# Kernel tuning notes

Measured on AMD Instinct MI355X. Metric: run time of the kernel, lower is better.

The kernel has to match this reference:

```python
import jax, jax.numpy as jnp
import numpy as np

EPS = 1e-6
K_MEM, C_MEM = 512, 2048
SEQ, BATCH = 256, 16
NUM_LAYERS, NUM_HEADS, HEAD_DIM = 12, 12, 64
KV_DIM = NUM_LAYERS * NUM_HEADS * HEAD_DIM * 2  # 18432
NOISE_STD = 0.01
PINV_STEPS = 3
BEN_COHEN_INIT = -5.0


def approx_pinv(A, steps=PINV_STEPS):
    # Ben-Cohen iterative pseudoinverse. A: (B, M, N) -> (B, N, M)
    alpha = jnp.minimum(jnp.exp(jnp.float32(BEN_COHEN_INIT)), jnp.float32(5e-4))  # clamp(max=5e-4)
    P = alpha * jnp.swapaxes(A, -2, -1)
    for _ in range(steps):
        P = 2.0 * P - (P @ A) @ P  # matches bmm(bmm(P, A), P)
    return P


def setup_inputs() -> dict:
    key = jax.random.key(0)
    ks = jax.random.split(key, 6)
    lim = np.sqrt(6.0 / (C_MEM + KV_DIM))  # xavier_uniform
    return {
        "z_sequence": jax.random.normal(ks[0], (SEQ, BATCH, C_MEM), jnp.float32),
        "z_query": jax.random.normal(ks[1], (BATCH, C_MEM), jnp.float32),
        "noise": jax.random.normal(ks[2], (SEQ, BATCH, C_MEM), jnp.float32),
        "memory_mean": jax.random.normal(ks[3], (K_MEM, C_MEM), jnp.float32) * 0.02,
        "memory_logvar": jnp.zeros((K_MEM,), jnp.float32),
        "w_logvar": jnp.zeros((1,), jnp.float32),
        "W_M_weight": jax.random.uniform(ks[4], (KV_DIM, C_MEM), jnp.float32, -lim, lim),
    }


def reference(z_sequence, z_query, noise, memory_mean, memory_logvar, w_logvar, W_M_weight):
    B = z_query.shape[0]
    # ---- write ----
    prior_var = jnp.exp(memory_logvar) + EPS                     # (K,)
    prior_mean_b = jnp.broadcast_to(memory_mean, (B, K_MEM, C_MEM))
    z_noise = z_sequence + noise * NOISE_STD                     # (S, B, C)
    z_t = jnp.swapaxes(z_noise, 0, 1)                            # (B, S, C)
    M_pinv = approx_pinv(prior_mean_b)                           # (B, C, K)
    w = z_t @ M_pinv                                             # (B, S, K)
    w_pinv = approx_pinv(w)                                      # (B, K, S)
    new_memory_mean = w_pinv @ z_t                               # (B, K, C)
    # KL divergence (post_var == prior_var here)
    t1 = C_MEM * jnp.sum(prior_var / prior_var)
    t2 = jnp.sum((new_memory_mean - prior_mean_b) ** 2 / prior_var[None, :, None], axis=(-2, -1))
    t3 = -jnp.float32(C_MEM * K_MEM)
    t4 = C_MEM * jnp.sum(jnp.log(prior_var) - jnp.log(prior_var))
    dkl_M = jnp.mean(t1 + t2 + t3 + t4)
    # ---- read (deterministic addressing) ----
    M_pinv2 = approx_pinv(new_memory_mean)                       # (B, C, K)
    w_mean = jnp.einsum('bc,bck->bk', z_query, M_pinv2)          # (B, K)
    z_retrieved = jnp.einsum('bk,bkc->bc', w_mean, new_memory_mean)  # (B, C)
    Z_r_kv = z_retrieved @ W_M_weight.T                          # (B, kv_dim)
    wl = jnp.broadcast_to(w_logvar, w_mean.shape)
    dkl_w = 0.5 * jnp.sum(jnp.exp(wl) + w_mean ** 2 - 1.0 - wl)
    return z_retrieved, Z_r_kv, dkl_M, dkl_w
```

## Files before the change

### kernel.cpp

```cpp
#include <hip/hip_runtime.h>

#define ALPHA 5.0e-4f

typedef short s16x8 __attribute__((ext_vector_type(8)));
typedef unsigned short u16x8 __attribute__((ext_vector_type(8)));
typedef unsigned short u16x4 __attribute__((ext_vector_type(4)));
typedef float f32x4 __attribute__((ext_vector_type(4)));

__device__ __forceinline__ unsigned short f2bf(float f) {
    unsigned int u = __builtin_bit_cast(unsigned int, f);
    u += 0x7fffu + ((u >> 16) & 1u);
    return (unsigned short)(u >> 16);
}
__device__ __forceinline__ float bf2f(unsigned short h) {
    return __builtin_bit_cast(float, (unsigned int)h << 16);
}
__device__ __forceinline__ f32x4 mfma16(s16x8 a, s16x8 b, f32x4 c) {
    return __builtin_amdgcn_mfma_f32_16x16x32_bf16(a, b, c, 0, 0, 0);
}

__device__ __forceinline__ void prefetch_chunk(const float* __restrict__ WM,
                                               int chunk, int tid)
{
    const float4* wp = (const float4*)WM + (long long)chunk * 12288;
    float4 s = {0.f, 0.f, 0.f, 0.f};
#pragma unroll 8
    for (int i = 0; i < 48; ++i) {
        const float4 v = wp[tid + i * 256];
        s.x += v.x; s.y += v.y; s.z += v.z; s.w += v.w;
    }
    asm volatile("" :: "v"(s.x), "v"(s.y), "v"(s.z), "v"(s.w));
}

template<int ROWS>
__device__ __forceinline__ void stage_kcontig(const float* __restrict__ src, int ld,
                                              unsigned short* __restrict__ lds, int tid)
{
#pragma unroll
    for (int it = 0; it < ROWS * 8 / 256; ++it) {
        const int g = tid + it * 256;
        const int row = g >> 3, s = g & 7;
        const float* p = src + (long long)row * ld + s * 8;
        const float4 x0 = *(const float4*)p;
        const float4 x1 = *(const float4*)(p + 4);
        u16x8 h;
        h[0] = f2bf(x0.x); h[1] = f2bf(x0.y); h[2] = f2bf(x0.z); h[3] = f2bf(x0.w);
        h[4] = f2bf(x1.x); h[5] = f2bf(x1.y); h[6] = f2bf(x1.z); h[7] = f2bf(x1.w);
        *(u16x8*)(lds + row * 64 + ((s ^ (row & 7)) << 3)) = h;
    }
}

template<int ROWS>
__device__ __forceinline__ void stage_kstrided(const float* __restrict__ src, int ld,
                                               unsigned short* __restrict__ lds, int tid)
{
    constexpr int KPT = ROWS * 64 / 256;
    const int m = tid % ROWS, kb = (tid / ROWS) * KPT;
#pragma unroll
    for (int j8 = 0; j8 < KPT / 8; ++j8) {
        u16x8 h;
#pragma unroll
        for (int j = 0; j < 8; ++j)
            h[j] = f2bf(src[(long long)(kb + j8 * 8 + j) * ld + m]);
        const int s = (kb >> 3) + j8;
        *(u16x8*)(lds + m * 64 + ((s ^ (m & 7)) << 3)) = h;
    }
}

template<int ROWS>
__device__ __forceinline__ void stage_kcontig_b(const unsigned short* __restrict__ src, int ld,
                                                unsigned short* __restrict__ lds, int tid)
{
#pragma unroll
    for (int it = 0; it < ROWS * 8 / 256; ++it) {
        const int g = tid + it * 256;
        const int row = g >> 3, s = g & 7;
        const u16x8 h = *(const u16x8*)(src + (long long)row * ld + s * 8);
        *(u16x8*)(lds + row * 64 + ((s ^ (row & 7)) << 3)) = h;
    }
}

template<int ROWS>
__device__ __forceinline__ void stage_kstrided_b(const unsigned short* __restrict__ src, int ld,
                                                 unsigned short* __restrict__ lds, int tid)
{
    constexpr int KPT = ROWS * 64 / 256;
    const int m = tid % ROWS, kb = (tid / ROWS) * KPT;
#pragma unroll
    for (int j8 = 0; j8 < KPT / 8; ++j8) {
        u16x8 h;
#pragma unroll
        for (int j = 0; j < 8; ++j)
            h[j] = src[(long long)(kb + j8 * 8 + j) * ld + m];
        const int s = (kb >> 3) + j8;
        *(u16x8*)(lds + m * 64 + ((s ^ (m & 7)) << 3)) = h;
    }
}

template<int BM, int BN, bool TA, bool TB>
__device__ __forceinline__
void gemm_dev_f32(int bx, int by,
                  const float* __restrict__ A, int lda,
                  const float* __restrict__ B, int ldb,
                  float* __restrict__ D, int ldd, int Kd)
{
    constexpr int TWM = BM / 2, TWN = BN / 2;
    constexpr int FM = TWM / 16, FN = TWN / 16;
    __shared__ unsigned short As[BM * 64];
    __shared__ unsigned short Bs[BN * 64];

    const int tid = threadIdx.x;
    const int lane = tid & 63, w = tid >> 6;
    const int wm = w >> 1, wn = w & 1;
    const int lrow = lane & 15, lk = lane >> 4;
    const int m0 = by * BM, n0 = bx * BN;

    f32x4 acc[FM][FN];
#pragma unroll
    for (int i = 0; i < FM; ++i)
#pragma unroll
        for (int j = 0; j < FN; ++j) acc[i][j] = (f32x4){0.f, 0.f, 0.f, 0.f};

    for (int k0 = 0; k0 < Kd; k0 += 64) {
        if (!TA) stage_kcontig<BM>(A + (long long)m0 * lda + k0, lda, As, tid);
        else     stage_kstrided<BM>(A + (long long)k0 * lda + m0, lda, As, tid);
        if (TB)  stage_kcontig<BN>(B + (long long)n0 * ldb + k0, ldb, Bs, tid);
        else     stage_kstrided<BN>(B + (long long)k0 * ldb + n0, ldb, Bs, tid);
        __syncthreads();
#pragma unroll
        for (int kk = 0; kk < 2; ++kk) {
            s16x8 ah[FM], bh[FN];
#pragma unroll
            for (int i = 0; i < FM; ++i) {
                const int row = wm * TWM + i * 16 + lrow;
                const int s = kk * 4 + lk;
                ah[i] = *(const s16x8*)(As + row * 64 + ((s ^ (row & 7)) << 3));
            }
#pragma unroll
            for (int j = 0; j < FN; ++j) {
                const int col = wn * TWN + j * 16 + lrow;
                const int s = kk * 4 + lk;
                bh[j] = *(const s16x8*)(Bs + col * 64 + ((s ^ (col & 7)) << 3));
            }
#pragma unroll
            for (int i = 0; i < FM; ++i)
#pragma unroll
                for (int j = 0; j < FN; ++j)
                    acc[i][j] = mfma16(ah[i], bh[j], acc[i][j]);
        }
        __syncthreads();
    }

#pragma unroll
    for (int i = 0; i < FM; ++i)
#pragma unroll
        for (int j = 0; j < FN; ++j) {
            const int col = n0 + wn * TWN + j * 16 + lrow;
#pragma unroll
            for (int r = 0; r < 4; ++r) {
                const int row = m0 + wm * TWM + i * 16 + lk * 4 + r;
                D[(long long)row * ldd + col] = acc[i][j][r];
            }
        }
}

__global__ __launch_bounds__(256)
void fused_prep_kernel(const float* __restrict__ zs, const float* __restrict__ no,
                       const float* __restrict__ zq, const float* __restrict__ mm,
                       unsigned short* __restrict__ ztb, float* __restrict__ q,
                       float* __restrict__ Gp)
{
    const int blk = blockIdx.x, t = threadIdx.x;
    if (blk % 9 == 8) {
        const int g = blk / 9;
        const int ky = g & 7;
        const int tile = g >> 3;
        gemm_dev_f32<64, 64, false, true>(
            tile & 7, tile >> 3,
            mm + ky * 256, 2048, mm + ky * 256, 2048,
            Gp + (long long)ky * 262144, 512, 256);
    } else {
        const int bs = blk - blk / 9;
        const int b = bs >> 8, sI = bs & 255;
        const long long in = ((long long)sI * 16 + b) * 2048 + t * 8;
        const f32x4 z0 = __builtin_nontemporal_load((const f32x4*)(zs + in));
        const f32x4 z1 = __builtin_nontemporal_load((const f32x4*)(zs + in + 4));
        const f32x4 n0 = __builtin_nontemporal_load((const f32x4*)(no + in));
        const f32x4 n1 = __builtin_nontemporal_load((const f32x4*)(no + in + 4));
        float zf[8];
#pragma unroll
        for (int j = 0; j < 4; ++j) {
            zf[j]     = fmaf(0.01f, n0[j], z0[j]);
            zf[j + 4] = fmaf(0.01f, n1[j], z1[j]);
        }
        u16x8 o;
#pragma unroll
        for (int j = 0; j < 8; ++j) o[j] = f2bf(zf[j]);
        *(u16x8*)(ztb + ((long long)bs * 2048 + t * 8)) = o;
        const float4 q0 = *(const float4*)(zq + b * 2048 + t * 8);
        const float4 q1 = *(const float4*)(zq + b * 2048 + t * 8 + 4);
        float qa = zf[0] * q0.x + zf[1] * q0.y + zf[2] * q0.z + zf[3] * q0.w
                 + zf[4] * q1.x + zf[5] * q1.y + zf[6] * q1.z + zf[7] * q1.w;
        __shared__ float red[256];
        red[t] = qa; __syncthreads();
        for (int st = 128; st > 0; st >>= 1) { if (t < st) red[t] += red[t + st]; __syncthreads(); }
        if (t == 0) q[bs] = red[0];
    }
}

__global__ __launch_bounds__(256)
void vg_kernel(const unsigned short* __restrict__ ztb, const float* __restrict__ mm,
               const float* __restrict__ Gp, const float* __restrict__ WM,
               unsigned short* __restrict__ Vb, unsigned short* __restrict__ G1b,
               float* __restrict__ wmean, float* __restrict__ out)
{
    const int blk = blockIdx.x, tid = threadIdx.x;
    if (blk < 512) {
        constexpr int BM = 64, BN = 64, TWM = 32, TWN = 32, FM = 2, FN = 2;
        __shared__ unsigned short As[BM * 64];
        __shared__ unsigned short Bs[BN * 64];
        const int r = blk & 7, t = blk >> 3;
        const int by = r + 8 * (t & 7), bx = t >> 3;
        const int lane = tid & 63, w = tid >> 6;
        const int wm = w >> 1, wn = w & 1;
        const int lrow = lane & 15, lk = lane >> 4;
        const int m0 = by * BM, n0 = bx * BN;

        f32x4 acc[FM][FN];
#pragma unroll
        for (int i = 0; i < FM; ++i)
#pragma unroll
            for (int j = 0; j < FN; ++j) acc[i][j] = (f32x4){0.f, 0.f, 0.f, 0.f};

        for (int k0 = 0; k0 < 2048; k0 += 64) {
            stage_kcontig_b<BM>(ztb + (long long)m0 * 2048 + k0, 2048, As, tid);
            stage_kcontig<BN>(mm + (long long)n0 * 2048 + k0, 2048, Bs, tid);
            __syncthreads();
#pragma unroll
            for (int kk = 0; kk < 2; ++kk) {
                s16x8 ah[FM], bh[FN];
#pragma unroll
                for (int i = 0; i < FM; ++i) {
                    const int row = wm * TWM + i * 16 + lrow;
                    const int s = kk * 4 + lk;
                    ah[i] = *(const s16x8*)(As + row * 64 + ((s ^ (row & 7)) << 3));
                }
#pragma unroll
                for (int j = 0; j < FN; ++j) {
                    const int col = wn * TWN + j * 16 + lrow;
                    const int s = kk * 4 + lk;
                    bh[j] = *(const s16x8*)(Bs + col * 64 + ((s ^ (col & 7)) << 3));
                }
#pragma unroll
                for (int i = 0; i < FM; ++i)
#pragma unroll
                    for (int j = 0; j < FN; ++j)
                        acc[i][j] = mfma16(ah[i], bh[j], acc[i][j]);
            }
            __syncthreads();
        }

#pragma unroll
        for (int i = 0; i < FM; ++i)
#pragma unroll
            for (int j = 0; j < FN; ++j) {
                const int col = n0 + wn * TWN + j * 16 + lrow;
#pragma unroll
                for (int rr = 0; rr < 4; ++rr) {
                    const int row = m0 + wm * TWM + i * 16 + lk * 4 + rr;
                    Vb[(long long)row * 512 + col] = f2bf(acc[i][j][rr]);
                }
            }
    } else if (blk < 768) {
        const int idx = (blk - 512) * 256 + tid;
        f32x4 s = {0.f, 0.f, 0.f, 0.f};
#pragma unroll
        for (int p = 0; p < 8; ++p) {
            const f32x4 v = *(const f32x4*)(Gp + (long long)p * 262144 + idx * 4);
            s[0] += v[0]; s[1] += v[1]; s[2] += v[2]; s[3] += v[3];
        }
        u16x4 h;
#pragma unroll
        for (int j = 0; j < 4; ++j) h[j] = f2bf(s[j]);
        *(u16x4*)(G1b + idx * 4) = h;
    } else if (blk < 777) {
        const int zb = blk - 768;
        float4* oz = (float4*)(out + 32768);
        const int base = (zb * 256 + tid) * 32;
#pragma unroll
        for (int i = 0; i < 32; ++i) oz[base + i] = (float4){0.f, 0.f, 0.f, 0.f};
        if (zb == 0) {
            float4* wm4 = (float4*)wmean;
            for (int i = tid; i < 2048; i += 256) wm4[i] = (float4){0.f, 0.f, 0.f, 0.f};
            if (tid == 0) out[327680] = 0.f;
        }
    } else {
        prefetch_chunk(WM, blk - 777, tid);
    }
}

__global__ __launch_bounds__(256)
void wT2_kernel(const unsigned short* __restrict__ Vb,
                const unsigned short* __restrict__ G1b,
                unsigned short* __restrict__ wTb,
                const float* __restrict__ q, float* __restrict__ wmean)
{
    constexpr int BM = 64, BN = 64, TWM = 32, TWN = 32, FM = 2, FN = 2;
    __shared__ unsigned short As[BM * 64];
    __shared__ unsigned short Bs[BN * 64];
    const int lin = blockIdx.x;
    const int r = lin & 7, t = lin >> 3;
    const int by = r + 8 * (t & 7), bx = t >> 3;
    const int tid = threadIdx.x;
    const int lane = tid & 63, w = tid >> 6;
    const int wm = w >> 1, wn = w & 1;
    const int lrow = lane & 15, lk = lane >> 4;
    const int m0 = by * BM, n0 = bx * BN;

    f32x4 acc[FM][FN];
#pragma unroll
    for (int i = 0; i < FM; ++i)
#pragma unroll
        for (int j = 0; j < FN; ++j) acc[i][j] = (f32x4){0.f, 0.f, 0.f, 0.f};

    for (int k0 = 0; k0 < 512; k0 += 64) {
        stage_kcontig_b<BM>(Vb + (long long)m0 * 512 + k0, 512, As, tid);
        stage_kcontig_b<BN>(G1b + (long long)n0 * 512 + k0, 512, Bs, tid);
        __syncthreads();
#pragma unroll
        for (int kk = 0; kk < 2; ++kk) {
            s16x8 ah[FM], bh[FN];
#pragma unroll
            for (int i = 0; i < FM; ++i) {
                const int row = wm * TWM + i * 16 + lrow;
                const int s = kk * 4 + lk;
                ah[i] = *(const s16x8*)(As + row * 64 + ((s ^ (row & 7)) << 3));
            }
#pragma unroll
            for (int j = 0; j < FN; ++j) {
                const int col = wn * TWN + j * 16 + lrow;
                const int s = kk * 4 + lk;
                bh[j] = *(const s16x8*)(Bs + col * 64 + ((s ^ (col & 7)) << 3));
            }
#pragma unroll
            for (int i = 0; i < FM; ++i)
#pragma unroll
                for (int j = 0; j < FN; ++j)
                    acc[i][j] = mfma16(ah[i], bh[j], acc[i][j]);
        }
        __syncthreads();
    }

    const float a8 = 8.0f * ALPHA, a28 = -28.0f * ALPHA * ALPHA;
    float up[FN] = {0.f, 0.f};
#pragma unroll
    for (int i = 0; i < FM; ++i)
#pragma unroll
        for (int rr = 0; rr < 4; ++rr) {
            const int row = m0 + wm * TWM + i * 16 + lk * 4 + rr;
            const float qv = q[row];
#pragma unroll
            for (int j = 0; j < FN; ++j) {
                const int col = n0 + wn * TWN + j * 16 + lrow;
                const float v = fmaf(a8, bf2f(Vb[(long long)row * 512 + col]),
                                     a28 * acc[i][j][rr]);
                wTb[(long long)(row >> 8) * 131072 + (long long)col * 256 + (row & 255)] = f2bf(v);
                up[j] = fmaf(v, qv, up[j]);
            }
        }
    const int b = m0 >> 8;
#pragma unroll
    for (int j = 0; j < FN; ++j) {
        float v = up[j];
        v += __shfl_xor(v, 16);
        v += __shfl_xor(v, 32);
        if (lk == 0) {
            const int col = n0 + wn * TWN + j * 16 + lrow;
            atomicAdd(&wmean[b * 512 + col], (64.0f * ALPHA * ALPHA) * v);
        }
    }
}

__global__ __launch_bounds__(256)
void tail1_kernel(const unsigned short* __restrict__ wTb,
                  const unsigned short* __restrict__ ztb,
                  const float* __restrict__ wmean, const float* __restrict__ wlv,
                  const float* __restrict__ WM, float* __restrict__ out)
{
    __shared__ __align__(16) float smemf[1024];
    const int blk = blockIdx.x, tid = threadIdx.x;
    if (blk < 256) {
        float* wms = smemf;
        float* ys  = smemf + 512;
        float* red2 = smemf + 768;
        const int r8 = blk & 7, t8 = blk >> 3;
        const int b = r8 + 8 * (t8 & 1), ct = t8 >> 1;
        wms[tid] = wmean[b * 512 + tid];
        wms[tid + 256] = wmean[b * 512 + 256 + tid];
        __syncthreads();
        {
            const unsigned short* wp = wTb + (long long)b * 131072 + tid;
            float yv = 0.f;
#pragma unroll 8
            for (int k = 0; k < 512; ++k)
                yv = fmaf(wms[k], bf2f(wp[(long long)k * 256]), yv);
            ys[tid] = yv;
        }
        __syncthreads();
        const int c = ct * 128 + (tid & 127), sh = tid >> 7;
        const unsigned short* zp = ztb + (long long)b * 524288 + c;
        float acc2 = 0.f;
        const int sbase = sh * 128;
#pragma unroll 8
        for (int s = 0; s < 128; ++s)
            acc2 = fmaf(ys[sbase + s], bf2f(zp[(long long)(sbase + s) * 2048]), acc2);
        red2[tid] = acc2; __syncthreads();
        if (sh == 0)
            out[(long long)b * 2048 + c] = (8.0f * ALPHA) * (red2[tid] + red2[tid + 128]);
    } else if (blk == 256) {
        float* red = smemf;
        float s = 0.f;
        for (int i = tid; i < 16 * 512; i += 256) { const float v = wmean[i]; s += v * v; }
        red[tid] = s; __syncthreads();
        for (int st = 128; st > 0; st >>= 1) { if (tid < st) red[tid] += red[tid + st]; __syncthreads(); }
        if (tid == 0) {
            const float l = wlv[0];
            out[327681] = 0.5f * (red[0] + 8192.0f * (expf(l) - 1.0f - l));
        }
    } else {
        prefetch_chunk(WM, 512 + (blk - 257), tid);
    }
}

__global__ __launch_bounds__(256)
void tail2_kernel(const unsigned short* __restrict__ wTb,
                  const unsigned short* __restrict__ ztb,
                  const float* __restrict__ mm, const float* __restrict__ mlv,
                  const float* __restrict__ WM, float* __restrict__ out)
{
    __shared__ __align__(16) unsigned char smem[34304];
    const int g = blockIdx.x, tid = threadIdx.x;
    const int grp = g / 26, p = g % 26;
    if (p < 8) {
        constexpr int BM = 128, BN = 128, TWM = 64, TWN = 64, FM = 4, FN = 4;
        unsigned short* As = (unsigned short*)smem;
        unsigned short* Bs = As + BM * 64;
        float* ivars = (float*)(smem + 32768);
        float* red = (float*)(smem + 33280);
        const int bz = ((2 * grp + p) & 7) + 8 * (grp & 1);
        const int rest = grp >> 1;
        const int by = rest & 3, bx = rest >> 2;
        const int lane = tid & 63, w = tid >> 6;
        const int wm = w >> 1, wn = w & 1;
        const int lrow = lane & 15, lk = lane >> 4;
        const int m0 = by * BM, n0 = bx * BN;

        if (tid < 128) ivars[tid] = 1.0f / (expf(mlv[m0 + tid]) + 1e-6f);

        f32x4 acc[FM][FN];
#pragma unroll
        for (int i = 0; i < FM; ++i)
#pragma unroll
            for (int j = 0; j < FN; ++j) acc[i][j] = (f32x4){0.f, 0.f, 0.f, 0.f};

        for (int k0 = 0; k0 < 256; k0 += 64) {
            stage_kcontig_b<BM>(wTb + (long long)bz * 131072 + (long long)m0 * 256 + k0, 256, As, tid);
            stage_kstrided_b<BN>(ztb + (long long)bz * 524288 + (long long)k0 * 2048 + n0, 2048, Bs, tid);
            __syncthreads();
#pragma unroll
            for (int kk = 0; kk < 2; ++kk) {
                s16x8 ah[FM], bh[FN];
#pragma unroll
                for (int i = 0; i < FM; ++i) {
                    const int row = wm * TWM + i * 16 + lrow;
                    const int s = kk * 4 + lk;
                    ah[i] = *(const s16x8*)(As + row * 64 + ((s ^ (row & 7)) << 3));
                }
#pragma unroll
                for (int j = 0; j < FN; ++j) {
                    const int col = wn * TWN + j * 16 + lrow;
                    const int s = kk * 4 + lk;
                    bh[j] = *(const s16x8*)(Bs + col * 64 + ((s ^ (col & 7)) << 3));
                }
#pragma unroll
                for (int i = 0; i < FM; ++i)
#pragma unroll
                    for (int j = 0; j < FN; ++j)
                        acc[i][j] = mfma16(ah[i], bh[j], acc[i][j]);
            }
            __syncthreads();
        }

        const float A8 = 8.0f * ALPHA;
        float da = 0.f;
#pragma unroll
        for (int i = 0; i < FM; ++i)
#pragma unroll
            for (int j = 0; j < FN; ++j) {
                const int cl = wn * TWN + j * 16 + lrow;
#pragma unroll
                for (int rr = 0; rr < 4; ++rr) {
                    const int rl = wm * TWM + i * 16 + lk * 4 + rr;
                    const float v = A8 * acc[i][j][rr];
                    const float d = v - mm[(long long)(m0 + rl) * 2048 + (n0 + cl)];
                    da = fmaf(d * d, ivars[rl], da);
                }
            }
        red[tid] = da; __syncthreads();
        for (int st = 128; st > 0; st >>= 1) { if (tid < st) red[tid] += red[tid + st]; __syncthreads(); }
        if (tid == 0) atomicAdd(&out[327680], red[0] * (1.0f / 16.0f));
    } else {
        const int z = grp * 18 + (p - 8);
        const int bx = z % 288, ky = z / 288;
        const int lane = tid & 63, w = tid >> 6;
        const int d0 = bx * 64 + w * 16;
        const int kc0 = ky * 256;
        const int rr = lane & 15, kq = lane >> 4;
        const float* zr = out;
        s16x8 areg[8];
        const float* zb = zr + rr * 2048 + kc0 + kq * 8;
#pragma unroll
        for (int s = 0; s < 8; ++s) {
            const f32x4 a0 = *(const f32x4*)(zb + s * 32);
            const f32x4 a1 = *(const f32x4*)(zb + s * 32 + 4);
            u16x8 h;
#pragma unroll
            for (int j = 0; j < 4; ++j) { h[j] = f2bf(a0[j]); h[j + 4] = f2bf(a1[j]); }
            areg[s] = __builtin_bit_cast(s16x8, h);
        }
        f32x4 acc = {0.f, 0.f, 0.f, 0.f};
        const float* wb = WM + (long long)(d0 + rr) * 2048 + kc0 + kq * 8;
#pragma unroll
        for (int s = 0; s < 8; ++s) {
            const f32x4 b0 = *(const f32x4*)(wb + s * 32);
            const f32x4 b1 = *(const f32x4*)(wb + s * 32 + 4);
            u16x8 h;
#pragma unroll
            for (int j = 0; j < 4; ++j) { h[j] = f2bf(b0[j]); h[j + 4] = f2bf(b1[j]); }
            acc = mfma16(areg[s], __builtin_bit_cast(s16x8, h), acc);
        }
        float* oz = out + 32768;
#pragma unroll
        for (int r = 0; r < 4; ++r)
            atomicAdd(&oz[(long long)(kq * 4 + r) * 18432 + d0 + rr], acc[r]);
    }
}

extern "C" void kernel_launch(void* const* d_in, const int* in_sizes, int n_in,
                              void* d_out, int out_size, void* d_ws, size_t ws_size,
                              hipStream_t stream)
{
    (void)in_sizes; (void)n_in; (void)out_size; (void)ws_size;
    const float* z_seq   = (const float*)d_in[0];
    const float* z_query = (const float*)d_in[1];
    const float* noise   = (const float*)d_in[2];
    const float* mm      = (const float*)d_in[3];
    const float* mlv     = (const float*)d_in[4];
    const float* wlv     = (const float*)d_in[5];
    const float* WM      = (const float*)d_in[6];
    float* out = (float*)d_out;

    char* wsb = (char*)d_ws;
    unsigned short* ztb  = (unsigned short*)(wsb);
    unsigned short* wTb  = (unsigned short*)(wsb + (16LL << 20));
    float*          Gp   = (float*)(wsb + (24LL << 20));
    unsigned short* G1b  = (unsigned short*)(wsb + (32LL << 20));
    unsigned short* Vb   = (unsigned short*)(wsb + (33LL << 20));
    float*          qvec = (float*)(wsb + (38LL << 20));
    float*          wmean = (float*)(wsb + (39LL << 20));

    fused_prep_kernel<<<4608, 256, 0, stream>>>(z_seq, noise, z_query, mm,
                                                ztb, qvec, Gp);
    vg_kernel<<<1289, 256, 0, stream>>>(ztb, mm, Gp, WM, Vb, G1b, wmean, out);
    wT2_kernel<<<512, 256, 0, stream>>>(Vb, G1b, wTb, qvec, wmean);
    tail1_kernel<<<513, 256, 0, stream>>>(wTb, ztb, wmean, wlv, WM, out);
    tail2_kernel<<<3328, 256, 0, stream>>>(wTb, ztb, mm, mlv, WM, out);
}
```

Measured before the change: 160.0 us.

## Compute w_mean algebraically from V and G1 to fuse wT GEMM with retrieval

Instead of waiting for the full wT matrix before computing w_mean, w_mean is derived from the product u=V^T q, which vg_kernel now accumulates with atomics. A small mid_kernel then applies G1 to get w_mean, the KL term, and a vector h. This lets the wT GEMM and the first retrieval projection (now V·h, computed from V directly) run concurrently in one launch, taking the wT→tail1 dependency off the critical path. In exchange it adds a small, poorly parallel 16-block kernel and changes floating-point summation order.

```diff
diff --git a/kernel.cpp b/kernel.cpp
--- a/kernel.cpp
+++ b/kernel.cpp
@@ -168,9 +168,14 @@
 void fused_prep_kernel(const float* __restrict__ zs, const float* __restrict__ no,
                        const float* __restrict__ zq, const float* __restrict__ mm,
                        unsigned short* __restrict__ ztb, float* __restrict__ q,
-                       float* __restrict__ Gp)
+                       float* __restrict__ Gp, float* __restrict__ uVb)
 {
     const int blk = blockIdx.x, t = threadIdx.x;
+    if (blk == 4608) {
+        float4* u4 = (float4*)uVb;
+        for (int i = t; i < 2048; i += 256) u4[i] = (float4){0.f, 0.f, 0.f, 0.f};
+        return;
+    }
     if (blk % 9 == 8) {
         const int g = blk / 9;
         const int ky = g & 7;
@@ -211,8 +216,9 @@
 __global__ __launch_bounds__(256)
 void vg_kernel(const unsigned short* __restrict__ ztb, const float* __restrict__ mm,
                const float* __restrict__ Gp, const float* __restrict__ WM,
+               const float* __restrict__ q,
                unsigned short* __restrict__ Vb, unsigned short* __restrict__ G1b,
-               float* __restrict__ wmean, float* __restrict__ out)
+               float* __restrict__ uVb, float* __restrict__ out)
 {
     const int blk = blockIdx.x, tid = threadIdx.x;
     if (blk < 512) {
@@ -260,17 +266,32 @@
             __syncthreads();
         }
 
+        float up[FN] = {0.f, 0.f};
 #pragma unroll
         for (int i = 0; i < FM; ++i)
 #pragma unroll
-            for (int j = 0; j < FN; ++j) {
+            for (int rr = 0; rr < 4; ++rr) {
+                const int row = m0 + wm * TWM + i * 16 + lk * 4 + rr;
+                const float qv = q[row];
+#pragma unroll
+                for (int j = 0; j < FN; ++j) {
+                    const int col = n0 + wn * TWN + j * 16 + lrow;
+                    const float v = acc[i][j][rr];
+                    Vb[(long long)row * 512 + col] = f2bf(v);
+                    up[j] = fmaf(v, qv, up[j]);
+                }
+            }
+        const int b = m0 >> 8;
+#pragma unroll
+        for (int j = 0; j < FN; ++j) {
+            float v = up[j];
+            v += __shfl_xor(v, 16);
+            v += __shfl_xor(v, 32);
+            if (lk == 0) {
                 const int col = n0 + wn * TWN + j * 16 + lrow;
-#pragma unroll
-                for (int rr = 0; rr < 4; ++rr) {
-                    const int row = m0 + wm * TWM + i * 16 + lk * 4 + rr;
-                    Vb[(long long)row * 512 + col] = f2bf(acc[i][j][rr]);
-                }
-            }
+                atomicAdd(&uVb[b * 512 + col], v);
+            }
+        }
     } else if (blk < 768) {
         const int idx = (blk - 512) * 256 + tid;
         f32x4 s = {0.f, 0.f, 0.f, 0.f};
@@ -289,122 +310,152 @@
         const int base = (zb * 256 + tid) * 32;
 #pragma unroll
         for (int i = 0; i < 32; ++i) oz[base + i] = (float4){0.f, 0.f, 0.f, 0.f};
-        if (zb == 0) {
-            float4* wm4 = (float4*)wmean;
-            for (int i = tid; i < 2048; i += 256) wm4[i] = (float4){0.f, 0.f, 0.f, 0.f};
-            if (tid == 0) out[327680] = 0.f;
-        }
+        if (zb == 0 && tid == 0) { out[327680] = 0.f; out[327681] = 0.f; }
     } else {
         prefetch_chunk(WM, blk - 777, tid);
     }
 }
 
+__global__ __launch_bounds__(512)
+void mid_kernel(const unsigned short* __restrict__ G1b, const float* __restrict__ uVb,
+                const float* __restrict__ wlv, float* __restrict__ hbuf,
+                float* __restrict__ out)
+{
+    __shared__ float uVs[512], wms[512], red[512];
+    const int b = blockIdx.x, k = threadIdx.x;
+    uVs[k] = uVb[b * 512 + k];
+    __syncthreads();
+    const unsigned short* grow = G1b + (long long)k * 512;
+    float g1 = 0.f;
+#pragma unroll 4
+    for (int j = 0; j < 512; j += 8) {
+        const u16x8 gv = *(const u16x8*)(grow + j);
+#pragma unroll
+        for (int jj = 0; jj < 8; ++jj) g1 = fmaf(bf2f(gv[jj]), uVs[j + jj], g1);
+    }
+    const float a8 = 8.0f * ALPHA, a28 = 28.0f * ALPHA * ALPHA;
+    const float wmk = (64.0f * ALPHA * ALPHA) * fmaf(-a28, g1, a8 * uVs[k]);
+    wms[k] = wmk;
+    red[k] = wmk * wmk;
+    __syncthreads();
+    for (int st = 256; st > 0; st >>= 1) { if (k < st) red[k] += red[k + st]; __syncthreads(); }
+    if (k == 0) {
+        float extra = 0.f;
+        if (b == 0) { const float l = wlv[0]; extra = 8192.0f * (expf(l) - 1.0f - l); }
+        atomicAdd(&out[327681], 0.5f * (red[0] + extra));
+    }
+    float g2 = 0.f;
+#pragma unroll 4
+    for (int j = 0; j < 512; j += 8) {
+        const u16x8 gv = *(const u16x8*)(grow + j);
+#pragma unroll
+        for (int jj = 0; jj < 8; ++jj) g2 = fmaf(bf2f(gv[jj]), wms[j + jj], g2);
+    }
+    hbuf[b * 512 + k] = fmaf(-a28, g2, a8 * wmk);
+}
+
 __global__ __launch_bounds__(256)
-void wT2_kernel(const unsigned short* __restrict__ Vb,
-                const unsigned short* __restrict__ G1b,
-                unsigned short* __restrict__ wTb,
-                const float* __restrict__ q, float* __restrict__ wmean)
-{
-    constexpr int BM = 64, BN = 64, TWM = 32, TWN = 32, FM = 2, FN = 2;
-    __shared__ unsigned short As[BM * 64];
-    __shared__ unsigned short Bs[BN * 64];
-    const int lin = blockIdx.x;
-    const int r = lin & 7, t = lin >> 3;
-    const int by = r + 8 * (t & 7), bx = t >> 3;
-    const int tid = threadIdx.x;
-    const int lane = tid & 63, w = tid >> 6;
-    const int wm = w >> 1, wn = w & 1;
-    const int lrow = lane & 15, lk = lane >> 4;
-    const int m0 = by * BM, n0 = bx * BN;
-
-    f32x4 acc[FM][FN];
-#pragma unroll
-    for (int i = 0; i < FM; ++i)
-#pragma unroll
-        for (int j = 0; j < FN; ++j) acc[i][j] = (f32x4){0.f, 0.f, 0.f, 0.f};
-
-    for (int k0 = 0; k0 < 512; k0 += 64) {
-        stage_kcontig_b<BM>(Vb + (long long)m0 * 512 + k0, 512, As, tid);
-        stage_kcontig_b<BN>(G1b + (long long)n0 * 512 + k0, 512, Bs, tid);
+void tail1b_kernel(const unsigned short* __restrict__ Vb,
+                   const unsigned short* __restrict__ G1b,
+                   const unsigned short* __restrict__ ztb,
+                   const float* __restrict__ hbuf, const float* __restrict__ WM,
+                   unsigned short* __restrict__ wTb, float* __restrict__ out)
+{
+    __shared__ __align__(16) unsigned char smem[36864];
+    const int blk = blockIdx.x, tid = threadIdx.x;
+    if (blk < 512) {
+        constexpr int BM = 64, BN = 64, TWM = 32, TWN = 32, FM = 2, FN = 2;
+        unsigned short* As = (unsigned short*)smem;
+        unsigned short* Bs = As + BM * 64;
+        const int r = blk & 7, t = blk >> 3;
+        const int by = r + 8 * (t & 7), bx = t >> 3;
+        const int lane = tid & 63, w = tid >> 6;
+        const int wm = w >> 1, wn = w & 1;
+        const int lrow = lane & 15, lk = lane >> 4;
+        const int m0 = by * BM, n0 = bx * BN;
+
+        f32x4 acc[FM][FN];
+#pragma unroll
+        for (int i = 0; i < FM; ++i)
+#pragma unroll
+            for (int j = 0; j < FN; ++j) acc[i][j] = (f32x4){0.f, 0.f, 0.f, 0.f};
+
+        for (int k0 = 0; k0 < 512; k0 += 64) {
+            stage_kcontig_b<BM>(Vb + (long long)m0 * 512 + k0, 512, As, tid);
+            stage_kcontig_b<BN>(G1b + (long long)n0 * 512 + k0, 512, Bs, tid);
+            __syncthreads();
+#pragma unroll
+            for (int kk = 0; kk < 2; ++kk) {
+                s16x8 ah[FM], bh[FN];
+#pragma unroll
+                for (int i = 0; i < FM; ++i) {
+                    const int row = wm * TWM + i * 16 + lrow;
+                    const int s = kk * 4 + lk;
+                    ah[i] = *(const s16x8*)(As + row * 64 + ((s ^ (row & 7)) << 3));
+                }
+#pragma unroll
+                for (int j = 0; j < FN; ++j) {
+                    const int col = wn * TWN + j * 16 + lrow;
+                    const int s = kk * 4 + lk;
+                    bh[j] = *(const s16x8*)(Bs + col * 64 + ((s ^ (col & 7)) << 3));
+                }
+#pragma unroll
+                for (int i = 0; i < FM; ++i)
+#pragma unroll
+                    for (int j = 0; j < FN; ++j)
+                        acc[i][j] = mfma16(ah[i], bh[j], acc[i][j]);
+            }
+            __syncthreads();
+        }
+
+        const float a8 = 8.0f * ALPHA, a28 = -28.0f * ALPHA * ALPHA;
+#pragma unroll
+        for (int i = 0; i < FM; ++i)
+#pragma unroll
+            for (int rr = 0; rr < 4; ++rr) {
+                const int row = m0 + wm * TWM + i * 16 + lk * 4 + rr;
+#pragma unroll
+                for (int j = 0; j < FN; ++j) {
+                    const int col = n0 + wn * TWN + j * 16 + lrow;
+                    const float v = fmaf(a8, bf2f(Vb[(long long)row * 512 + col]),
+                                         a28 * acc[i][j][rr]);
+                    wTb[(long long)(row >> 8) * 131072 + (long long)col * 256 + (row & 255)] = f2bf(v);
+                }
+            }
+    } else if (blk < 768) {
+        unsigned short* Vt = (unsigned short*)smem;
+        float* hs  = (float*)(smem + 32768);
+        float* ys  = (float*)(smem + 34816);
+        float* red2 = (float*)(smem + 35840);
+        const int idx = blk - 512;
+        const int r8 = idx & 7, t8 = idx >> 3;
+        const int b = r8 + 8 * (t8 & 1), ct = t8 >> 1;
+        hs[tid] = hbuf[b * 512 + tid];
+        hs[tid + 256] = 0.f;
+        hs[tid + 256] = hbuf[b * 512 + 256 + tid];
         __syncthreads();
-#pragma unroll
-        for (int kk = 0; kk < 2; ++kk) {
-            s16x8 ah[FM], bh[FN];
-#pragma unroll
-            for (int i = 0; i < FM; ++i) {
-                const int row = wm * TWM + i * 16 + lrow;
-                const int s = kk * 4 + lk;
-                ah[i] = *(const s16x8*)(As + row * 64 + ((s ^ (row & 7)) << 3));
-            }
-#pragma unroll
-            for (int j = 0; j < FN; ++j) {
-                const int col = wn * TWN + j * 16 + lrow;
-                const int s = kk * 4 + lk;
-                bh[j] = *(const s16x8*)(Bs + col * 64 + ((s ^ (col & 7)) << 3));
-            }
-#pragma unroll
-            for (int i = 0; i < FM; ++i)
-#pragma unroll
-                for (int j = 0; j < FN; ++j)
-                    acc[i][j] = mfma16(ah[i], bh[j], acc[i][j]);
-        }
-        __syncthreads();
-    }
-
-    const float a8 = 8.0f * ALPHA, a28 = -28.0f * ALPHA * ALPHA;
-    float up[FN] = {0.f, 0.f};
-#pragma unroll
-    for (int i = 0; i < FM; ++i)
-#pragma unroll
-        for (int rr = 0; rr < 4; ++rr) {
-            const int row = m0 + wm * TWM + i * 16 + lk * 4 + rr;
-            const float qv = q[row];
-#pragma unroll
-            for (int j = 0; j < FN; ++j) {
-                const int col = n0 + wn * TWN + j * 16 + lrow;
-                const float v = fmaf(a8, bf2f(Vb[(long long)row * 512 + col]),
-                                     a28 * acc[i][j][rr]);
-                wTb[(long long)(row >> 8) * 131072 + (long long)col * 256 + (row & 255)] = f2bf(v);
-                up[j] = fmaf(v, qv, up[j]);
-            }
-        }
-    const int b = m0 >> 8;
-#pragma unroll
-    for (int j = 0; j < FN; ++j) {
-        float v = up[j];
-        v += __shfl_xor(v, 16);
-        v += __shfl_xor(v, 32);
-        if (lk == 0) {
-            const int col = n0 + wn * TWN + j * 16 + lrow;
-            atomicAdd(&wmean[b * 512 + col], (64.0f * ALPHA * ALPHA) * v);
-        }
-    }
-}
-
-__global__ __launch_bounds__(256)
-void tail1_kernel(const unsigned short* __restrict__ wTb,
-                  const unsigned short* __restrict__ ztb,
-                  const float* __restrict__ wmean, const float* __restrict__ wlv,
-                  const float* __restrict__ WM, float* __restrict__ out)
-{
-    __shared__ __align__(16) float smemf[1024];
-    const int blk = blockIdx.x, tid = threadIdx.x;
-    if (blk < 256) {
-        float* wms = smemf;
-        float* ys  = smemf + 512;
-        float* red2 = smemf + 768;
-        const int r8 = blk & 7, t8 = blk >> 3;
-        const int b = r8 + 8 * (t8 & 1), ct = t8 >> 1;
-        wms[tid] = wmean[b * 512 + tid];
-        wms[tid + 256] = wmean[b * 512 + 256 + tid];
-        __syncthreads();
-        {
-            const unsigned short* wp = wTb + (long long)b * 131072 + tid;
-            float yv = 0.f;
-#pragma unroll 8
-            for (int k = 0; k < 512; ++k)
-                yv = fmaf(wms[k], bf2f(wp[(long long)k * 256]), yv);
-            ys[tid] = yv;
+        const int sl = tid >> 3, grp = tid & 7;
+        for (int t = 0; t < 8; ++t) {
+            __syncthreads();
+#pragma unroll
+            for (int i = 0; i < 8; ++i) {
+                const int e = tid + i * 256;
+                const int row = e >> 6, s8 = e & 63;
+                const u16x8 v = *(const u16x8*)(Vb + ((long long)(b * 256 + t * 32 + row)) * 512 + s8 * 8);
+                *(u16x8*)(Vt + row * 512 + ((s8 ^ (row & 7)) << 3)) = v;
+            }
+            __syncthreads();
+            float p = 0.f;
+#pragma unroll
+            for (int j = 0; j < 8; ++j) {
+                const int slot = (grp * 8 + j) ^ (sl & 7);
+                const u16x8 v = *(const u16x8*)(Vt + sl * 512 + slot * 8);
+                const int kb = grp * 64 + j * 8;
+#pragma unroll
+                for (int jj = 0; jj < 8; ++jj) p = fmaf(bf2f(v[jj]), hs[kb + jj], p);
+            }
+            p += __shfl_xor(p, 1); p += __shfl_xor(p, 2); p += __shfl_xor(p, 4);
+            if (grp == 0) ys[t * 32 + sl] = p;
         }
         __syncthreads();
         const int c = ct * 128 + (tid & 127), sh = tid >> 7;
@@ -417,18 +468,8 @@
         red2[tid] = acc2; __syncthreads();
         if (sh == 0)
             out[(long long)b * 2048 + c] = (8.0f * ALPHA) * (red2[tid] + red2[tid + 128]);
-    } else if (blk == 256) {
-        float* red = smemf;
-        float s = 0.f;
-        for (int i = tid; i < 16 * 512; i += 256) { const float v = wmean[i]; s += v * v; }
-        red[tid] = s; __syncthreads();
-        for (int st = 128; st > 0; st >>= 1) { if (tid < st) red[tid] += red[tid + st]; __syncthreads(); }
-        if (tid == 0) {
-            const float l = wlv[0];
-            out[327681] = 0.5f * (red[0] + 8192.0f * (expf(l) - 1.0f - l));
-        }
     } else {
-        prefetch_chunk(WM, 512 + (blk - 257), tid);
+        prefetch_chunk(WM, 512 + (blk - 768), tid);
     }
 }
 
@@ -567,12 +608,13 @@
     unsigned short* G1b  = (unsigned short*)(wsb + (32LL << 20));
     unsigned short* Vb   = (unsigned short*)(wsb + (33LL << 20));
     float*          qvec = (float*)(wsb + (38LL << 20));
-    float*          wmean = (float*)(wsb + (39LL << 20));
-
-    fused_prep_kernel<<<4608, 256, 0, stream>>>(z_seq, noise, z_query, mm,
-                                                ztb, qvec, Gp);
-    vg_kernel<<<1289, 256, 0, stream>>>(ztb, mm, Gp, WM, Vb, G1b, wmean, out);
-    wT2_kernel<<<512, 256, 0, stream>>>(Vb, G1b, wTb, qvec, wmean);
-    tail1_kernel<<<513, 256, 0, stream>>>(wTb, ztb, wmean, wlv, WM, out);
+    float*          uVb  = (float*)(wsb + (39LL << 20));
+    float*          hbuf = (float*)(wsb + (40LL << 20));
+
+    fused_prep_kernel<<<4609, 256, 0, stream>>>(z_seq, noise, z_query, mm,
+                                                ztb, qvec, Gp, uVb);
+    vg_kernel<<<1289, 256, 0, stream>>>(ztb, mm, Gp, WM, qvec, Vb, G1b, uVb, out);
+    mid_kernel<<<16, 512, 0, stream>>>(G1b, uVb, wlv, hbuf, out);
+    tail1b_kernel<<<1024, 256, 0, stream>>>(Vb, G1b, ztb, hbuf, WM, wTb, out);
     tail2_kernel<<<3328, 256, 0, stream>>>(wTb, ztb, mm, mlv, WM, out);
 }
```

Result: slower. 184.2 us (+15.1%).
